# Kernel tuning notes

Hardware: AMD Instinct MI355X
Metric: run time of the kernel (lower is better)

Reference implementation:

```python
import jax, jax.numpy as jnp
import numpy as np
import math

B, S, H, NH = 8, 2048, 256, 4
DH = H // NH
EPS = 1e-12


def setup_inputs() -> dict:
    key = jax.random.key(0)
    ks = jax.random.split(key, 20)
    g = lambda k, shape: (jax.random.normal(k, shape, jnp.float32) * 0.02)
    inp = {
        "hidden": jax.random.normal(ks[0], (B, S, H), jnp.float32),
        "Wq": g(ks[1], (H, H)), "bq": jnp.zeros((H,), jnp.float32),
        "Wk": g(ks[2], (H, H)), "bk": jnp.zeros((H,), jnp.float32),
        "Wv": g(ks[3], (H, H)), "bv": jnp.zeros((H,), jnp.float32),
        "Wo": g(ks[4], (H, H)), "bo": jnp.zeros((H,), jnp.float32),
        "W1": g(ks[5], (4 * H, H)), "b1": jnp.zeros((4 * H,), jnp.float32),
        "W2": g(ks[6], (H, 4 * H)), "b2": jnp.zeros((H,), jnp.float32),
        "ln1_w": jnp.ones((H,), jnp.float32), "ln1_b": jnp.zeros((H,), jnp.float32),
        "ln2_w": jnp.ones((H,), jnp.float32), "ln2_b": jnp.zeros((H,), jnp.float32),
        "mask": jax.random.randint(ks[7], (B, S), 0, 2, jnp.int32),
    }
    return inp


def _layernorm(x, w, b):
    u = x.mean(-1, keepdims=True)
    s = ((x - u) ** 2).mean(-1, keepdims=True)
    return w * (x - u) / jnp.sqrt(s + EPS) + b


def _gelu_tanh(h):
    return 0.5 * h * (1.0 + jnp.tanh(math.sqrt(2.0 / math.pi) * (h + 0.044715 * h ** 3)))


def _block(hidden, mask, Wq, bq, Wk, bk, Wv, bv, Wo, bo, W1, b1, W2, b2,
           ln1_w, ln1_b, ln2_w, ln2_b):
    # --- attention sublayer (pre-norm + residual) ---
    x = _layernorm(hidden, ln1_w, ln1_b)
    def heads(W, b):  # [B,S,H] -> [B,NH,S,DH]
        return (x @ W.T + b).reshape(B, S, NH, DH).transpose(0, 2, 1, 3)
    q, k, v = heads(Wq, bq), heads(Wk, bk), heads(Wv, bv)
    corr = jnp.einsum("bhqd,bhkd->bhqk", q, k) / math.sqrt(DH)
    # torch code masks QUERY rows: mask [B,S] broadcast over heads and keys
    corr = jnp.where(mask[:, None, :, None] == 0, -1e9, corr)
    prob = jax.nn.softmax(corr, axis=-1)
    attn = jnp.einsum("bhqk,bhkd->bhqd", prob, v)
    attn = attn.transpose(0, 2, 1, 3).reshape(B, S, H) @ Wo.T + bo
    hidden = hidden + attn
    # --- FFN sublayer (pre-norm + residual) ---
    y = _layernorm(hidden, ln2_w, ln2_b)
    h1 = y @ W1.T + b1
    ff = _gelu_tanh(h1) @ W2.T + b2
    return hidden + ff


def reference(hidden, Wq, bq, Wk, bk, Wv, bv, Wo, bo, W1, b1, W2, b2,
              ln1_w, ln1_b, ln2_w, ln2_b, mask):
    return _block(hidden, mask, Wq, bq, Wk, bk, Wv, bv, Wo, bo,
                  W1, b1, W2, b2, ln1_w, ln1_b, ln2_w, ln2_b)
```

## Files before the change

### kernel.cpp

```cpp
#include <hip/hip_runtime.h>
#include <hip/hip_bf16.h>
#include <cstdint>
#include <cstddef>

constexpr int CB  = 8;
constexpr int CS  = 2048;
constexpr int CH  = 256;
constexpr int CNH = 4;
constexpr int CDH = 64;
constexpr int CT  = CB * CS;

typedef __attribute__((ext_vector_type(8)))  __bf16 bf16x8;
typedef __attribute__((ext_vector_type(4)))  float  f32x4;
typedef __attribute__((ext_vector_type(16))) float  f32x16;
typedef __attribute__((ext_vector_type(2)))  int    i32x2;

__device__ __forceinline__ float b2f(unsigned short u) {
    union { float f; unsigned int i; } v; v.i = ((unsigned int)u) << 16; return v.f;
}
__device__ __forceinline__ unsigned short f2b(float f) {
    union { float f; unsigned int i; } v; v.f = f;
    unsigned int r = v.i + 0x7FFFu + ((v.i >> 16) & 1u);
    return (unsigned short)(r >> 16);
}
__device__ __forceinline__ unsigned int packbf(float a, float b) {
    float2 t; t.x = a; t.y = b;
    __hip_bfloat162 h = __float22bfloat162_rn(t);
    union { __hip_bfloat162 h; unsigned int u; } c; c.h = h; return c.u;
}
__device__ __forceinline__ float fexp2(float x) {
#if __has_builtin(__builtin_amdgcn_exp2f)
    return __builtin_amdgcn_exp2f(x);
#else
    float r; asm("v_exp_f32 %0, %1" : "=v"(r) : "v"(x)); return r;
#endif
}
__device__ __forceinline__ f32x4 mfma16(bf16x8 a, bf16x8 b, f32x4 c) {
    return __builtin_amdgcn_mfma_f32_16x16x32_bf16(a, b, c, 0, 0, 0);
}
__device__ __forceinline__ f32x16 mfma32(bf16x8 a, bf16x8 b, f32x16 c) {
    return __builtin_amdgcn_mfma_f32_32x32x16_bf16(a, b, c, 0, 0, 0);
}
__device__ __forceinline__ f32x16 zero16() {
    f32x16 z;
    #pragma unroll
    for (int i = 0; i < 16; ++i) z[i] = 0.f;
    return z;
}

#define GLOAD_LDS16(gptr, lptr)                                                        \
    __builtin_amdgcn_global_load_lds((const __attribute__((address_space(1))) void*)(gptr), \
                                     (__attribute__((address_space(3))) void*)(lptr), 16, 0, 0)

#define QSCALE 0.1803368801111204f

__global__ __launch_bounds__(256) void detect_kernel(
    const unsigned short* __restrict__ h, int* __restrict__ flag)
{
    __shared__ int s_bad;
    const int tid = threadIdx.x;
    if (tid == 0) s_bad = 0;
    __syncthreads();
    bool bad = false;
    for (int i = tid; i < 2048; i += 256) {
        float v = b2f(h[i]);
        if (!(fabsf(v) < 1e25f)) bad = true;
    }
    if (bad) s_bad = 1;
    __syncthreads();
    if (tid == 0) *flag = s_bad;
}

struct CvtW { const void* src[7]; void* dst[7]; int n[7]; };
struct CvtB { const void* src[10]; void* dst[10]; int n[10]; };

__global__ __launch_bounds__(256) void cvt_wb_k(const int* __restrict__ flag, CvtW a)
{
    const int seg = blockIdx.y, n = a.n[seg];
    const bool inf32 = (*flag != 0);
    const float* sf = (const float*)a.src[seg];
    const unsigned short* sb = (const unsigned short*)a.src[seg];
    unsigned short* d = (unsigned short*)a.dst[seg];
    for (int i = (blockIdx.x * 256 + threadIdx.x) * 4; i < n; i += gridDim.x * 1024) {
        ushort4 o;
        if (inf32) {
            float4 v = *(const float4*)(sf + i);
            o.x = f2b(v.x); o.y = f2b(v.y); o.z = f2b(v.z); o.w = f2b(v.w);
        } else {
            o = *(const ushort4*)(sb + i);
        }
        *(ushort4*)(d + i) = o;
    }
}

__global__ __launch_bounds__(256) void cvt_bf_k(const int* __restrict__ flag, CvtB a)
{
    const int seg = blockIdx.y, n = a.n[seg];
    const bool inf32 = (*flag != 0);
    const float* sf = (const float*)a.src[seg];
    const unsigned short* sb = (const unsigned short*)a.src[seg];
    float* d = (float*)a.dst[seg];
    const int i = threadIdx.x * 4;
    if (i < n) {
        float4 o;
        if (inf32) {
            o = *(const float4*)(sf + i);
        } else {
            ushort4 v = *(const ushort4*)(sb + i);
            o.x = b2f(v.x); o.y = b2f(v.y); o.z = b2f(v.z); o.w = b2f(v.w);
        }
        *(float4*)(d + i) = o;
    }
}

__global__ __launch_bounds__(256) void ln_kernel(
    const unsigned short* __restrict__ x, const float* __restrict__ w,
    const float* __restrict__ b, unsigned short* __restrict__ out)
{
    const int wave = threadIdx.x >> 6, lane = threadIdx.x & 63;
    const int token = blockIdx.x * 4 + wave;
    const int c = lane * 4;
    const size_t rowo = (size_t)token * CH + c;
    ushort4 u = *(const ushort4*)(x + rowo);
    float v0 = b2f(u.x), v1 = b2f(u.y), v2 = b2f(u.z), v3 = b2f(u.w);
    float s = v0 + v1 + v2 + v3;
    float q = v0*v0 + v1*v1 + v2*v2 + v3*v3;
    #pragma unroll
    for (int m = 1; m < 64; m <<= 1) { s += __shfl_xor(s, m, 64); q += __shfl_xor(q, m, 64); }
    float mean = s * (1.0f/256.0f);
    float var  = q * (1.0f/256.0f) - mean*mean;
    float inv  = rsqrtf(var + 1e-12f);
    float4 ww = *(const float4*)(w + c);
    float4 bb = *(const float4*)(b + c);
    ushort4 o;
    o.x = f2b(ww.x * (v0-mean)*inv + bb.x);
    o.y = f2b(ww.y * (v1-mean)*inv + bb.y);
    o.z = f2b(ww.z * (v2-mean)*inv + bb.z);
    o.w = f2b(ww.w * (v3-mean)*inv + bb.w);
    *(ushort4*)(out + rowo) = o;
}

template<bool GELU, bool RESID, bool HEADSTORE, bool OUTDYN>
__device__ __forceinline__ void gemm_core(
    const unsigned short* __restrict__ A, const unsigned short* __restrict__ W,
    const float* __restrict__ bias, const unsigned short* __restrict__ resid,
    void* __restrict__ out, const int* __restrict__ flag,
    int K, int N, int m0, int n0, float oscale)
{
    __shared__ __align__(16) unsigned short lA[2][128*32];
    __shared__ __align__(16) unsigned short lB[2][128*32];
    const int tid  = threadIdx.x;
    const int lane = tid & 63;
    const int wave = tid >> 6;
    const int wr = (wave >> 1) * 64;
    const int wc = (wave & 1) * 64;
    const int g = lane >> 4, r16 = lane & 15;
    const int lrow = lane >> 2;
    const int lch  = lane & 3;

#define GSTAGE(BUF, K0) do {                                                            \
        _Pragma("unroll")                                                               \
        for (int i = 0; i < 2; ++i) {                                                   \
            int chunk = wave + i * 4;                \
            int row = chunk * 16 + lrow;                                                \
            const unsigned short* ga = A + (size_t)(m0 + row) * K + (K0) + lch * 8;     \
            GLOAD_LDS16(ga, &lA[BUF][chunk * 512]);                                     \
            const unsigned short* gw = W + (size_t)(n0 + row) * K + (K0) + lch * 8;     \
            GLOAD_LDS16(gw, &lB[BUF][chunk * 512]);                                     \
        } } while (0)

    const f32x4 zero = {0.f, 0.f, 0.f, 0.f};
    f32x4 acc[4][4];
    #pragma unroll
    for (int m = 0; m < 4; ++m)
        #pragma unroll
        for (int n = 0; n < 4; ++n) acc[m][n] = zero;

    GSTAGE(0, 0);
    __syncthreads();
    const int NT = K >> 5;
    for (int t = 0; t < NT; ++t) {
        const int cur = t & 1;
        if (t + 1 < NT) GSTAGE(cur ^ 1, (t + 1) * 32);
        bf16x8 af[4], wf[4];
        #pragma unroll
        for (int m = 0; m < 4; ++m) af[m] = *(const bf16x8*)&lA[cur][(wr + m*16 + r16) * 32 + g * 8];
        #pragma unroll
        for (int n = 0; n < 4; ++n) wf[n] = *(const bf16x8*)&lB[cur][(wc + n*16 + r16) * 32 + g * 8];
        __builtin_amdgcn_s_setprio(1);
        #pragma unroll
        for (int m = 0; m < 4; ++m)
            #pragma unroll
            for (int n = 0; n < 4; ++n)
                acc[m][n] = mfma16(af[m], wf[n], acc[m][n]);
        __builtin_amdgcn_s_setprio(0);
        __syncthreads();
    }
#undef GSTAGE

    const bool of32dyn = OUTDYN ? (*flag != 0) : false;
    #pragma unroll
    for (int n = 0; n < 4; ++n) {
        int col = n0 + wc + n*16 + r16;
        float bv = bias[col];
        #pragma unroll
        for (int m = 0; m < 4; ++m) {
            int row0 = m0 + wr + m*16 + g*4;
            #pragma unroll
            for (int r = 0; r < 4; ++r) {
                int row = row0 + r;
                float v = (acc[m][n][r] + bv) * oscale;
                if (GELU) {
                    float a = 0.79788456080286541f * (v + 0.044715f * v * v * v);
                    v = v * (1.0f / (1.0f + __expf(-2.0f * a)));
                }
                if (RESID) v += b2f(resid[(size_t)row * N + col]);
                size_t oidx;
                if (HEADSTORE) {
                    int hh = col >> 6, d = col & 63;
                    int bb = row >> 11, ss = row & 2047;
                    oidx = ((((size_t)bb * CNH + hh) * CS) + ss) * CDH + d;
                } else {
                    oidx = (size_t)row * N + col;
                }
                if (OUTDYN && of32dyn) ((float*)out)[oidx] = v;
                else                   ((unsigned short*)out)[oidx] = f2b(v);
            }
        }
    }
}

__global__ __launch_bounds__(256) void k_qkv(
    const unsigned short* __restrict__ xhat,
    const unsigned short* Wq, const float* bq, unsigned short* q,
    const unsigned short* Wk, const float* bk, unsigned short* k,
    const unsigned short* Wv, const float* bv, unsigned short* v)
{
    const unsigned short* W  = blockIdx.z == 0 ? Wq : (blockIdx.z == 1 ? Wk : Wv);
    const float*          bi = blockIdx.z == 0 ? bq : (blockIdx.z == 1 ? bk : bv);
    unsigned short*       o  = blockIdx.z == 0 ? q  : (blockIdx.z == 1 ? k  : v);
    const float osc = blockIdx.z == 0 ? QSCALE : 1.0f;
    gemm_core<false, false, true, false>(xhat, W, bi, nullptr, o, nullptr,
                                         CH, CH, blockIdx.x * 128, blockIdx.y * 128, osc);
}

__global__ __launch_bounds__(256) void k_oproj(
    const unsigned short* __restrict__ A, const unsigned short* __restrict__ W,
    const float* __restrict__ bias, const unsigned short* __restrict__ resid,
    unsigned short* __restrict__ out)
{
    gemm_core<false, true, false, false>(A, W, bias, resid, out, nullptr,
                                         CH, CH, blockIdx.x * 128, blockIdx.y * 128, 1.0f);
}

__global__ __launch_bounds__(256) void k_ffn1(
    const unsigned short* __restrict__ A, const unsigned short* __restrict__ W,
    const float* __restrict__ bias, unsigned short* __restrict__ out)
{
    gemm_core<true, false, false, false>(A, W, bias, nullptr, out, nullptr,
                                         CH, 4*CH, blockIdx.x * 128, blockIdx.y * 128, 1.0f);
}

__global__ __launch_bounds__(256) void k_ffn2(
    const unsigned short* __restrict__ A, const unsigned short* __restrict__ W,
    const float* __restrict__ bias, const unsigned short* __restrict__ resid,
    void* __restrict__ out, const int* __restrict__ flag)
{
    gemm_core<false, true, false, true>(A, W, bias, resid, out, flag,
                                        4*CH, CH, blockIdx.x * 128, blockIdx.y * 128, 1.0f);
}

__global__ __launch_bounds__(256) void vtrans_kernel(
    const unsigned short* __restrict__ v, unsigned short* __restrict__ vt)
{
    __shared__ unsigned short T[64 * 72];
    const int bh = blockIdx.y, s0 = blockIdx.x * 64, tid = threadIdx.x;
    const size_t ibase = (size_t)bh * CS * CDH;
    const size_t obase = (size_t)bh * CDH * CS;
    #pragma unroll
    for (int i = 0; i < 2; ++i) {
        int t2 = tid + i * 256;
        int row = t2 >> 3, ch = t2 & 7;
        uint4 dv = *(const uint4*)(v + ibase + (size_t)(s0 + row) * CDH + ch * 8);
        *(uint4*)&T[row * 72 + ch * 8] = dv;
    }
    __syncthreads();
    #pragma unroll
    for (int i = 0; i < 2; ++i) {
        int t2 = tid + i * 256;
        int d = t2 >> 3, ch = t2 & 7;
        unsigned short tmp[8];
        #pragma unroll
        for (int j = 0; j < 8; ++j) tmp[j] = T[(ch * 8 + j) * 72 + d];
        *(uint4*)(vt + obase + (size_t)d * CS + s0 + ch * 8) = *(uint4*)tmp;
    }
}

__global__ __launch_bounds__(512, 4) void attn_kernel(
    const unsigned short* __restrict__ Q, const unsigned short* __restrict__ Kp,
    const unsigned short* __restrict__ Vt, const int* __restrict__ mask,
    unsigned short* __restrict__ out)
{
    __shared__ __align__(16) char lds[65536];

    const int tid = threadIdx.x, lane = tid & 63, wave = tid >> 6;
    const int qb = wave >> 1, kh = wave & 1;
    const int r32 = lane & 31, hi = lane >> 5;
    const int bh = blockIdx.y, bb = bh >> 2, hh = bh & 3;
    const int q0 = blockIdx.x * 128;
    const size_t baseQ = (size_t)bh * CS * CDH;
    const size_t baseT = (size_t)bh * CDH * CS;

    const int qrow = q0 + qb * 32 + r32;
    bf16x8 qf[4];
    {
        const bool live = (mask[bb * CS + qrow] != 0);
        #pragma unroll
        for (int dw = 0; dw < 4; ++dw) {
            uint4 v = {0u, 0u, 0u, 0u};
            if (live) v = *(const uint4*)(Q + baseQ + (size_t)qrow * CDH + dw * 16 + hi * 8);
            qf[dw] = *(bf16x8*)&v;
        }
    }

#define STAGE(BUF, KT) do {                                                             \
        _Pragma("unroll")                                                               \
        for (int i = 0; i < 2; ++i) {                                                   \
            const int slot0 = i * 512 + wave * 64;                                      \
            const int slot  = slot0 + lane;                                             \
            const int kw = slot >> 7, kk2 = slot & 127;                                 \
            GLOAD_LDS16(Kp + baseQ + (size_t)((KT) + kk2) * CDH + kw * 8,               \
                        lds + (BUF) * 16384 + slot0 * 16);                              \
            const int vc = slot >> 6, vd = slot & 63;                                   \
            GLOAD_LDS16(Vt + baseT + (size_t)vd * CS + (KT) + vc * 8,                   \
                        lds + 32768 + (BUF) * 16384 + slot0 * 16);                      \
        } } while (0)

    f32x16 o0 = zero16(), o1 = zero16();
    float psum = 0.f;

    STAGE(0, 0);
    __syncthreads();

    for (int t = 0; t < CS / 128; ++t) {
        const int buf = t & 1;
        const int kt = t * 128;
        if (t + 1 < CS / 128) STAGE(buf ^ 1, kt + 128);

        const char* kbase = lds + buf * 16384;
        const char* vbase = lds + 32768 + buf * 16384;

        f32x16 sT0 = zero16(), sT1 = zero16();
        __builtin_amdgcn_s_setprio(1);
        #pragma unroll
        for (int dw = 0; dw < 4; ++dw) {
            const char* cb = kbase + (dw * 2 + hi) * 2048;
            bf16x8 k0 = *(const bf16x8*)(cb + (kh * 64 + r32) * 16);
            bf16x8 k1 = *(const bf16x8*)(cb + (kh * 64 + 32 + r32) * 16);
            sT0 = mfma32(k0, qf[dw], sT0);
            sT1 = mfma32(k1, qf[dw], sT1);
        }
        __builtin_amdgcn_s_setprio(0);

#define PROCKB(SREG, KB) do {                                                           \
            float p[16];                                                                \
            _Pragma("unroll")                                                           \
            for (int r = 0; r < 16; ++r) { p[r] = fexp2((SREG)[r]); psum += p[r]; }     \
            _Pragma("unroll")                                                           \
            for (int w = 0; w < 2; ++w) {                                               \
                unsigned int a01 = packbf(p[w*8+0], p[w*8+1]);                          \
                unsigned int a23 = packbf(p[w*8+2], p[w*8+3]);                          \
                unsigned int b01 = packbf(p[w*8+4], p[w*8+5]);                          \
                unsigned int b23 = packbf(p[w*8+6], p[w*8+7]);                          \
                unsigned int ap0, ap1, ap2, ap3;                                        \
                {                                                                       \
                    i32x2 s1 = __builtin_amdgcn_permlane32_swap((int)a01, (int)b01, false, false); \
                    i32x2 s2 = __builtin_amdgcn_permlane32_swap((int)a23, (int)b23, false, false); \
                    ap0 = (unsigned int)s1.x; ap2 = (unsigned int)s1.y;                 \
                    ap1 = (unsigned int)s2.x; ap3 = (unsigned int)s2.y;                 \
                }                                                                       \
                union { unsigned int u[4]; bf16x8 v; } apv;                             \
                apv.u[0] = ap0; apv.u[1] = ap1; apv.u[2] = ap2; apv.u[3] = ap3;         \
                const char* vb2 = vbase + ((kh * 4 + (KB) * 2 + w) * 2 + hi) * 1024;    \
                bf16x8 v0 = *(const bf16x8*)(vb2 + r32 * 16);                           \
                bf16x8 v1 = *(const bf16x8*)(vb2 + (32 + r32) * 16);                    \
                o0 = mfma32(apv.v, v0, o0);                                             \
                o1 = mfma32(apv.v, v1, o1);                                             \
            } } while (0)

        PROCKB(sT0, 0);
        PROCKB(sT1, 1);
#undef PROCKB

        __syncthreads();
    }

    float ps = psum + __shfl_xor(psum, 32, 64);
    float* lsum = (float*)(lds + 32768);
    float* Oex  = (float*)lds;
    if (lane < 32) lsum[(qb * 2 + kh) * 32 + r32] = ps;
    if (kh == 1) {
        #pragma unroll
        for (int r = 0; r < 16; ++r) {
            const int qr = (r & 3) + 8 * (r >> 2) + 4 * hi;
            Oex[(qb * 32 + qr) * 64 + r32]      = o0[r];
            Oex[(qb * 32 + qr) * 64 + 32 + r32] = o1[r];
        }
    }
    __syncthreads();
    if (kh == 0) {
        #pragma unroll
        for (int r = 0; r < 16; ++r) {
            const int qr = (r & 3) + 8 * (r >> 2) + 4 * hi;
            const float l = lsum[(qb * 2 + 0) * 32 + qr] + lsum[(qb * 2 + 1) * 32 + qr];
            const float inv = 1.0f / l;
            const float u0 = (o0[r] + Oex[(qb * 32 + qr) * 64 + r32]) * inv;
            const float u1 = (o1[r] + Oex[(qb * 32 + qr) * 64 + 32 + r32]) * inv;
            const size_t ob = (size_t)(bb * CS + q0 + qb * 32 + qr) * CH + hh * CDH;
            out[ob + r32]      = f2b(u0);
            out[ob + 32 + r32] = f2b(u1);
        }
    }
#undef STAGE
}

extern "C" void kernel_launch(void* const* d_in, const int* in_sizes, int n_in,
                              void* d_out, int out_size, void* d_ws, size_t ws_size,
                              hipStream_t stream)
{
    const void* hidden = d_in[0];
    const void* Wq = d_in[1];  const void* bq = d_in[2];
    const void* Wk = d_in[3];  const void* bk = d_in[4];
    const void* Wv = d_in[5];  const void* bv = d_in[6];
    const void* Wo = d_in[7];  const void* bo = d_in[8];
    const void* W1 = d_in[9];  const void* b1 = d_in[10];
    const void* W2 = d_in[11]; const void* b2 = d_in[12];
    const void* ln1w = d_in[13]; const void* ln1b = d_in[14];
    const void* ln2w = d_in[15]; const void* ln2b = d_in[16];
    const int* mask = (const int*)d_in[17];

    char* ws = (char*)d_ws;
    const size_t KB = 1u << 10, MB = 1u << 20;
    int*            flag  = (int*)ws;
    float*          bqf   = (float*)(ws + 4*KB);
    float*          bkf   = (float*)(ws + 8*KB);
    float*          bvf   = (float*)(ws + 12*KB);
    float*          bof   = (float*)(ws + 16*KB);
    float*          b1f   = (float*)(ws + 20*KB);
    float*          b2f_  = (float*)(ws + 28*KB);
    float*          ln1wf = (float*)(ws + 32*KB);
    float*          ln1bf = (float*)(ws + 36*KB);
    float*          ln2wf = (float*)(ws + 40*KB);
    float*          ln2bf = (float*)(ws + 44*KB);
    unsigned short* Wqb   = (unsigned short*)(ws + 1*MB);
    unsigned short* Wkb   = (unsigned short*)(ws + 1*MB + 256*KB);
    unsigned short* Wvb   = (unsigned short*)(ws + 1*MB + 512*KB);
    unsigned short* Wob   = (unsigned short*)(ws + 1*MB + 768*KB);
    unsigned short* W1b   = (unsigned short*)(ws + 2*MB);
    unsigned short* W2b   = (unsigned short*)(ws + 2*MB + 512*KB);
    unsigned short* hb16  = (unsigned short*)(ws + 3*MB);
    unsigned short* xhat  = (unsigned short*)(ws + 11*MB);
    unsigned short* qb    = (unsigned short*)(ws + 19*MB);
    unsigned short* kb    = (unsigned short*)(ws + 27*MB);
    unsigned short* vb    = (unsigned short*)(ws + 35*MB);
    unsigned short* vtb   = (unsigned short*)(ws + 43*MB);
    unsigned short* attnb = xhat;
    unsigned short* hid2b = qb;
    unsigned short* yhat  = kb;
    unsigned short* h1g   = (unsigned short*)(ws + 51*MB);

    dim3 blk(256);
    detect_kernel<<<1, blk, 0, stream>>>((const unsigned short*)hidden, flag);

    CvtW cw;
    cw.src[0]=Wq;  cw.dst[0]=Wqb;  cw.n[0]=CH*CH;
    cw.src[1]=Wk;  cw.dst[1]=Wkb;  cw.n[1]=CH*CH;
    cw.src[2]=Wv;  cw.dst[2]=Wvb;  cw.n[2]=CH*CH;
    cw.src[3]=Wo;  cw.dst[3]=Wob;  cw.n[3]=CH*CH;
    cw.src[4]=W1;  cw.dst[4]=W1b;  cw.n[4]=4*CH*CH;
    cw.src[5]=W2;  cw.dst[5]=W2b;  cw.n[5]=4*CH*CH;
    cw.src[6]=hidden; cw.dst[6]=hb16; cw.n[6]=CT*CH;
    cvt_wb_k<<<dim3(256, 7), blk, 0, stream>>>(flag, cw);

    CvtB cf;
    cf.src[0]=bq;    cf.dst[0]=bqf;   cf.n[0]=CH;
    cf.src[1]=bk;    cf.dst[1]=bkf;   cf.n[1]=CH;
    cf.src[2]=bv;    cf.dst[2]=bvf;   cf.n[2]=CH;
    cf.src[3]=bo;    cf.dst[3]=bof;   cf.n[3]=CH;
    cf.src[4]=b1;    cf.dst[4]=b1f;   cf.n[4]=4*CH;
    cf.src[5]=b2;    cf.dst[5]=b2f_;  cf.n[5]=CH;
    cf.src[6]=ln1w;  cf.dst[6]=ln1wf; cf.n[6]=CH;
    cf.src[7]=ln1b;  cf.dst[7]=ln1bf; cf.n[7]=CH;
    cf.src[8]=ln2w;  cf.dst[8]=ln2wf; cf.n[8]=CH;
    cf.src[9]=ln2b;  cf.dst[9]=ln2bf; cf.n[9]=CH;
    cvt_bf_k<<<dim3(1, 10), blk, 0, stream>>>(flag, cf);

    ln_kernel<<<CT / 4, blk, 0, stream>>>(hb16, ln1wf, ln1bf, xhat);
    k_qkv<<<dim3(CT / 128, CH / 128, 3), blk, 0, stream>>>(xhat, Wqb, bqf, qb,
                                                           Wkb, bkf, kb, Wvb, bvf, vb);
    vtrans_kernel<<<dim3(CS / 64, CB * CNH), blk, 0, stream>>>(vb, vtb);
    attn_kernel<<<dim3(CS / 128, CB * CNH), dim3(512), 0, stream>>>(qb, kb, vtb, mask, attnb);
    k_oproj<<<dim3(CT / 128, CH / 128), blk, 0, stream>>>(attnb, Wob, bof, hb16, hid2b);
    ln_kernel<<<CT / 4, blk, 0, stream>>>(hid2b, ln2wf, ln2bf, yhat);
    k_ffn1<<<dim3(CT / 128, (4 * CH) / 128), blk, 0, stream>>>(yhat, W1b, b1f, h1g);
    k_ffn2<<<dim3(CT / 128, CH / 128), blk, 0, stream>>>(h1g, W2b, b2f_, hid2b,
                                                         d_out, flag);
}
```

Baseline: 172.1 us.

## Restructure GEMM core to stage only weights in LDS and fuse V transpose

The GEMM core now loads only 128-wide K chunks of the weight tile into LDS, in a k-major layout. The activation fragments are read straight from global memory into registers, which drops the A-tile LDS double buffer and most per-32-K barriers. The QKV kernel writes V directly in transposed [d][s] layout with packed 4-element stores, so the separate vtrans kernel and its buffer round trip are gone. It also adds occupancy hints to launch_bounds and computes GELU with exp2, at the risk of less latency hiding for the direct global A loads.

```diff
diff --git a/kernel.cpp b/kernel.cpp
--- a/kernel.cpp
+++ b/kernel.cpp
@@ -140,34 +140,21 @@
     *(ushort4*)(out + rowo) = o;
 }
 
-template<bool GELU, bool RESID, bool HEADSTORE, bool OUTDYN>
+template<bool GELU, bool RESID, bool OUTDYN>
 __device__ __forceinline__ void gemm_core(
     const unsigned short* __restrict__ A, const unsigned short* __restrict__ W,
     const float* __restrict__ bias, const unsigned short* __restrict__ resid,
     void* __restrict__ out, const int* __restrict__ flag,
-    int K, int N, int m0, int n0, float oscale)
-{
-    __shared__ __align__(16) unsigned short lA[2][128*32];
-    __shared__ __align__(16) unsigned short lB[2][128*32];
+    int K, int N, int m0, int n0, float oscale, int storemode)
+{
+    __shared__ __align__(16) unsigned short lW[16 * 128 * 8];
+
     const int tid  = threadIdx.x;
     const int lane = tid & 63;
     const int wave = tid >> 6;
     const int wr = (wave >> 1) * 64;
     const int wc = (wave & 1) * 64;
     const int g = lane >> 4, r16 = lane & 15;
-    const int lrow = lane >> 2;
-    const int lch  = lane & 3;
-
-#define GSTAGE(BUF, K0) do {                                                            \
-        _Pragma("unroll")                                                               \
-        for (int i = 0; i < 2; ++i) {                                                   \
-            int chunk = wave + i * 4;                \
-            int row = chunk * 16 + lrow;                                                \
-            const unsigned short* ga = A + (size_t)(m0 + row) * K + (K0) + lch * 8;     \
-            GLOAD_LDS16(ga, &lA[BUF][chunk * 512]);                                     \
-            const unsigned short* gw = W + (size_t)(n0 + row) * K + (K0) + lch * 8;     \
-            GLOAD_LDS16(gw, &lB[BUF][chunk * 512]);                                     \
-        } } while (0)
 
     const f32x4 zero = {0.f, 0.f, 0.f, 0.f};
     f32x4 acc[4][4];
@@ -176,27 +163,33 @@
         #pragma unroll
         for (int n = 0; n < 4; ++n) acc[m][n] = zero;
 
-    GSTAGE(0, 0);
-    __syncthreads();
-    const int NT = K >> 5;
-    for (int t = 0; t < NT; ++t) {
-        const int cur = t & 1;
-        if (t + 1 < NT) GSTAGE(cur ^ 1, (t + 1) * 32);
-        bf16x8 af[4], wf[4];
-        #pragma unroll
-        for (int m = 0; m < 4; ++m) af[m] = *(const bf16x8*)&lA[cur][(wr + m*16 + r16) * 32 + g * 8];
-        #pragma unroll
-        for (int n = 0; n < 4; ++n) wf[n] = *(const bf16x8*)&lB[cur][(wc + n*16 + r16) * 32 + g * 8];
-        __builtin_amdgcn_s_setprio(1);
-        #pragma unroll
-        for (int m = 0; m < 4; ++m)
+    for (int c = 0; c < K; c += 128) {
+        if (c) __syncthreads();
+        #pragma unroll
+        for (int i = 0; i < 8; ++i) {
+            const int s0 = i * 256 + wave * 64;
+            const int s  = s0 + lane;
+            const int kw = s >> 7, row = s & 127;
+            GLOAD_LDS16(W + (size_t)(n0 + row) * K + c + kw * 8, (char*)lW + s0 * 16);
+        }
+        __syncthreads();
+        #pragma unroll
+        for (int kk = 0; kk < 4; ++kk) {
+            bf16x8 af[4], wf[4];
+            #pragma unroll
+            for (int m = 0; m < 4; ++m)
+                af[m] = *(const bf16x8*)(A + (size_t)(m0 + wr + m*16 + r16) * K
+                                           + c + kk * 32 + g * 8);
             #pragma unroll
             for (int n = 0; n < 4; ++n)
-                acc[m][n] = mfma16(af[m], wf[n], acc[m][n]);
-        __builtin_amdgcn_s_setprio(0);
-        __syncthreads();
-    }
-#undef GSTAGE
+                wf[n] = *(const bf16x8*)&lW[((kk*4 + g) * 128 + wc + n*16 + r16) * 8];
+            #pragma unroll
+            for (int m = 0; m < 4; ++m)
+                #pragma unroll
+                for (int n = 0; n < 4; ++n)
+                    acc[m][n] = mfma16(af[m], wf[n], acc[m][n]);
+        }
+    }
 
     const bool of32dyn = OUTDYN ? (*flag != 0) : false;
     #pragma unroll
@@ -206,31 +199,42 @@
         #pragma unroll
         for (int m = 0; m < 4; ++m) {
             int row0 = m0 + wr + m*16 + g*4;
-            #pragma unroll
-            for (int r = 0; r < 4; ++r) {
-                int row = row0 + r;
-                float v = (acc[m][n][r] + bv) * oscale;
-                if (GELU) {
-                    float a = 0.79788456080286541f * (v + 0.044715f * v * v * v);
-                    v = v * (1.0f / (1.0f + __expf(-2.0f * a)));
+            if (storemode == 2) {
+                ushort4 pk;
+                unsigned short* pp = (unsigned short*)&pk;
+                #pragma unroll
+                for (int r = 0; r < 4; ++r) pp[r] = f2b(acc[m][n][r] + bv);
+                const int hh = col >> 6, d = col & 63;
+                const int bb = row0 >> 11, ss = row0 & 2047;
+                *(ushort4*)((unsigned short*)out +
+                    (((size_t)(bb * CNH + hh)) * CDH + d) * CS + ss) = pk;
+            } else {
+                #pragma unroll
+                for (int r = 0; r < 4; ++r) {
+                    int row = row0 + r;
+                    float v = (acc[m][n][r] + bv) * oscale;
+                    if (GELU) {
+                        float a = 0.79788456080286541f * (v + 0.044715f * v * v * v);
+                        v = v * (1.0f / (1.0f + fexp2(a * -2.8853900817779268f)));
+                    }
+                    if (RESID) v += b2f(resid[(size_t)row * N + col]);
+                    size_t oidx;
+                    if (storemode == 1) {
+                        int hh = col >> 6, d = col & 63;
+                        int bb = row >> 11, ss = row & 2047;
+                        oidx = ((((size_t)bb * CNH + hh) * CS) + ss) * CDH + d;
+                    } else {
+                        oidx = (size_t)row * N + col;
+                    }
+                    if (OUTDYN && of32dyn) ((float*)out)[oidx] = v;
+                    else                   ((unsigned short*)out)[oidx] = f2b(v);
                 }
-                if (RESID) v += b2f(resid[(size_t)row * N + col]);
-                size_t oidx;
-                if (HEADSTORE) {
-                    int hh = col >> 6, d = col & 63;
-                    int bb = row >> 11, ss = row & 2047;
-                    oidx = ((((size_t)bb * CNH + hh) * CS) + ss) * CDH + d;
-                } else {
-                    oidx = (size_t)row * N + col;
-                }
-                if (OUTDYN && of32dyn) ((float*)out)[oidx] = v;
-                else                   ((unsigned short*)out)[oidx] = f2b(v);
             }
         }
     }
 }
 
-__global__ __launch_bounds__(256) void k_qkv(
+__global__ __launch_bounds__(256, 4) void k_qkv(
     const unsigned short* __restrict__ xhat,
     const unsigned short* Wq, const float* bq, unsigned short* q,
     const unsigned short* Wk, const float* bk, unsigned short* k,
@@ -240,60 +244,35 @@
     const float*          bi = blockIdx.z == 0 ? bq : (blockIdx.z == 1 ? bk : bv);
     unsigned short*       o  = blockIdx.z == 0 ? q  : (blockIdx.z == 1 ? k  : v);
     const float osc = blockIdx.z == 0 ? QSCALE : 1.0f;
-    gemm_core<false, false, true, false>(xhat, W, bi, nullptr, o, nullptr,
-                                         CH, CH, blockIdx.x * 128, blockIdx.y * 128, osc);
-}
-
-__global__ __launch_bounds__(256) void k_oproj(
+    const int sm = blockIdx.z == 2 ? 2 : 1;
+    gemm_core<false, false, false>(xhat, W, bi, nullptr, o, nullptr,
+                                   CH, CH, blockIdx.x * 128, blockIdx.y * 128, osc, sm);
+}
+
+__global__ __launch_bounds__(256, 4) void k_oproj(
     const unsigned short* __restrict__ A, const unsigned short* __restrict__ W,
     const float* __restrict__ bias, const unsigned short* __restrict__ resid,
     unsigned short* __restrict__ out)
 {
-    gemm_core<false, true, false, false>(A, W, bias, resid, out, nullptr,
-                                         CH, CH, blockIdx.x * 128, blockIdx.y * 128, 1.0f);
-}
-
-__global__ __launch_bounds__(256) void k_ffn1(
+    gemm_core<false, true, false>(A, W, bias, resid, out, nullptr,
+                                  CH, CH, blockIdx.x * 128, blockIdx.y * 128, 1.0f, 0);
+}
+
+__global__ __launch_bounds__(256, 4) void k_ffn1(
     const unsigned short* __restrict__ A, const unsigned short* __restrict__ W,
     const float* __restrict__ bias, unsigned short* __restrict__ out)
 {
-    gemm_core<true, false, false, false>(A, W, bias, nullptr, out, nullptr,
-                                         CH, 4*CH, blockIdx.x * 128, blockIdx.y * 128, 1.0f);
-}
-
-__global__ __launch_bounds__(256) void k_ffn2(
+    gemm_core<true, false, false>(A, W, bias, nullptr, out, nullptr,
+                                  CH, 4*CH, blockIdx.x * 128, blockIdx.y * 128, 1.0f, 0);
+}
+
+__global__ __launch_bounds__(256, 4) void k_ffn2(
     const unsigned short* __restrict__ A, const unsigned short* __restrict__ W,
     const float* __restrict__ bias, const unsigned short* __restrict__ resid,
     void* __restrict__ out, const int* __restrict__ flag)
 {
-    gemm_core<false, true, false, true>(A, W, bias, resid, out, flag,
-                                        4*CH, CH, blockIdx.x * 128, blockIdx.y * 128, 1.0f);
-}
-
-__global__ __launch_bounds__(256) void vtrans_kernel(
-    const unsigned short* __restrict__ v, unsigned short* __restrict__ vt)
-{
-    __shared__ unsigned short T[64 * 72];
-    const int bh = blockIdx.y, s0 = blockIdx.x * 64, tid = threadIdx.x;
-    const size_t ibase = (size_t)bh * CS * CDH;
-    const size_t obase = (size_t)bh * CDH * CS;
-    #pragma unroll
-    for (int i = 0; i < 2; ++i) {
-        int t2 = tid + i * 256;
-        int row = t2 >> 3, ch = t2 & 7;
-        uint4 dv = *(const uint4*)(v + ibase + (size_t)(s0 + row) * CDH + ch * 8);
-        *(uint4*)&T[row * 72 + ch * 8] = dv;
-    }
-    __syncthreads();
-    #pragma unroll
-    for (int i = 0; i < 2; ++i) {
-        int t2 = tid + i * 256;
-        int d = t2 >> 3, ch = t2 & 7;
-        unsigned short tmp[8];
-        #pragma unroll
-        for (int j = 0; j < 8; ++j) tmp[j] = T[(ch * 8 + j) * 72 + d];
-        *(uint4*)(vt + obase + (size_t)d * CS + s0 + ch * 8) = *(uint4*)tmp;
-    }
+    gemm_core<false, true, true>(A, W, bias, resid, out, flag,
+                                 4*CH, CH, blockIdx.x * 128, blockIdx.y * 128, 1.0f, 0);
 }
 
 __global__ __launch_bounds__(512, 4) void attn_kernel(
@@ -462,8 +441,7 @@
     unsigned short* xhat  = (unsigned short*)(ws + 11*MB);
     unsigned short* qb    = (unsigned short*)(ws + 19*MB);
     unsigned short* kb    = (unsigned short*)(ws + 27*MB);
-    unsigned short* vb    = (unsigned short*)(ws + 35*MB);
-    unsigned short* vtb   = (unsigned short*)(ws + 43*MB);
+    unsigned short* vtb   = (unsigned short*)(ws + 35*MB);
     unsigned short* attnb = xhat;
     unsigned short* hid2b = qb;
     unsigned short* yhat  = kb;
@@ -497,8 +475,7 @@
 
     ln_kernel<<<CT / 4, blk, 0, stream>>>(hb16, ln1wf, ln1bf, xhat);
     k_qkv<<<dim3(CT / 128, CH / 128, 3), blk, 0, stream>>>(xhat, Wqb, bqf, qb,
-                                                           Wkb, bkf, kb, Wvb, bvf, vb);
-    vtrans_kernel<<<dim3(CS / 64, CB * CNH), blk, 0, stream>>>(vb, vtb);
+                                                           Wkb, bkf, kb, Wvb, bvf, vtb);
     attn_kernel<<<dim3(CS / 128, CB * CNH), dim3(512), 0, stream>>>(qb, kb, vtb, mask, attnb);
     k_oproj<<<dim3(CT / 128, CH / 128), blk, 0, stream>>>(attnb, Wob, bof, hb16, hid2b);
     ln_kernel<<<CT / 4, blk, 0, stream>>>(hid2b, ln2wf, ln2bf, yhat);
```

Result: slower. 221.6 us (+28.8%).
